# Optimization experiments

Measured on AMD Instinct MI355X. Metric: run time of the kernel, lower is better.

## Reference

```python
import jax, jax.numpy as jnp
import numpy as np

B, N, C = 4, 2047, 1024
H = 16
D = C // H  # head_dim = 64
SCALE = D ** -0.5


def setup_inputs() -> dict:
    key = jax.random.key(0)
    ks = jax.random.split(key, 5)
    return {
        "x": jax.random.normal(ks[0], (B, N, C), dtype=jnp.float32),
        "qkv_w": jax.random.normal(ks[1], (3 * C, C), dtype=jnp.float32) * (C ** -0.5),
        "proj_w": jax.random.normal(ks[2], (C, C), dtype=jnp.float32) * (C ** -0.5),
        "proj_b": jax.random.normal(ks[3], (C,), dtype=jnp.float32) * 0.02,
        "bias": jax.random.normal(ks[4], (H, N, N), dtype=jnp.float32) * 0.02,
    }


def reference(x, qkv_w, proj_w, proj_b, bias):
    b, n, c = x.shape
    qkv = (x @ qkv_w.T).reshape(b, n, 3, H, D)
    qkv = jnp.transpose(qkv, (2, 0, 3, 1, 4))
    q, k, v = qkv[0], qkv[1], qkv[2]
    q = q * SCALE
    # scores (B,H,N,N) + additive relative-position bias (H,N,N)
    attn = jnp.einsum('bhnd,bhmd->bhnm', q, k) + bias[None]
    attn = jax.nn.softmax(attn, axis=-1)
    out = jnp.einsum('bhnm,bhmd->bhnd', attn, v)
    out = jnp.transpose(out, (0, 2, 1, 3)).reshape(b, n, c)
    return out @ proj_w.T + proj_b
```

## Files before the change

kernel.cpp:

```cpp
#include <hip/hip_runtime.h>
#include <hip/hip_bf16.h>

typedef __bf16 bf16;
typedef __attribute__((ext_vector_type(8))) __bf16 bf16x8;
typedef __attribute__((ext_vector_type(4))) __bf16 bf16x4;
typedef __attribute__((ext_vector_type(4))) float f32x4;

#define MFMA16(a, b, c) __builtin_amdgcn_mfma_f32_16x16x32_bf16((a), (b), (c), 0, 0, 0)

constexpr int Bb = 4, Nn = 2047, Cc = 1024, Hh = 16, Dd = 64;
constexpr int M_ROWS = Bb * Nn;
constexpr int NPAD = 2048;
constexpr float SCALE = 0.125f;
constexpr float NEG_BIG = -1e30f;

__device__ inline bf16x8 bzero8() {
    bf16x8 v;
    for (int i = 0; i < 8; ++i) v[i] = (bf16)0.0f;
    return v;
}
__device__ inline bf16x8 bones8() {
    bf16x8 v;
    for (int i = 0; i < 8; ++i) v[i] = (bf16)1.0f;
    return v;
}
__device__ inline f32x4 fzero4() {
    f32x4 v = {0.f, 0.f, 0.f, 0.f};
    return v;
}

__device__ __forceinline__ void async_copy16(const void* g, void* l) {
    __builtin_amdgcn_global_load_lds(
        (const __attribute__((address_space(1))) unsigned int*)g,
        (__attribute__((address_space(3))) unsigned int*)l, 16, 0, 0);
}

__global__ __launch_bounds__(256) void cvt3_kernel(
    const float* __restrict__ a, bf16* __restrict__ oa, int na8,
    const float* __restrict__ b, bf16* __restrict__ ob, int nb8,
    const float* __restrict__ c, bf16* __restrict__ oc, int nc8) {
    int i = blockIdx.x * blockDim.x + threadIdx.x;
    const float* src;
    bf16* dst;
    int j = i;
    if (j < na8) {
        src = a; dst = oa;
    } else {
        j -= na8;
        if (j < nb8) {
            src = b; dst = ob;
        } else {
            j -= nb8;
            if (j >= nc8) return;
            src = c; dst = oc;
        }
    }
    float4 x0 = ((const float4*)src)[2 * (size_t)j];
    float4 x1 = ((const float4*)src)[2 * (size_t)j + 1];
    bf16x8 v;
    v[0] = (bf16)x0.x; v[1] = (bf16)x0.y; v[2] = (bf16)x0.z; v[3] = (bf16)x0.w;
    v[4] = (bf16)x1.x; v[5] = (bf16)x1.y; v[6] = (bf16)x1.z; v[7] = (bf16)x1.w;
    *(bf16x8*)(dst + 8 * (size_t)j) = v;
}

__global__ __launch_bounds__(256) void transpose_v_kernel(
    const bf16* __restrict__ vd, bf16* __restrict__ vtd) {
    __shared__ bf16 t[64 * 72];
    const int bh = blockIdx.x, nt = blockIdx.y;
    const int tid = threadIdx.x;
    const bf16* src = vd + (size_t)bh * Nn * Dd;
    bf16* dst = vtd + (size_t)bh * Dd * NPAD;
    int c = tid;
    for (int it = 0; it < 2; ++it, c += 256) {
        int row = c >> 3, d8 = (c & 7) * 8;
        int gn = nt * 64 + row;
        bf16x8 v = bzero8();
        if (gn < Nn) v = *(const bf16x8*)(src + (size_t)gn * Dd + d8);
        *(bf16x8*)(t + row * 72 + d8) = v;
    }
    __syncthreads();
    c = tid;
    for (int it = 0; it < 2; ++it, c += 256) {
        int d = c >> 3, j8 = (c & 7) * 8;
        bf16x8 v;
        for (int k = 0; k < 8; ++k) v[k] = t[(j8 + k) * 72 + d];
        *(bf16x8*)(dst + (size_t)d * NPAD + nt * 64 + j8) = v;
    }
}

template <int NOUT, int MODE>
__global__ __launch_bounds__(256, 2) void gemm_kernel(
    const bf16* __restrict__ A, const bf16* __restrict__ W,
    const float* __restrict__ pb, bf16* __restrict__ qd, bf16* __restrict__ kd,
    bf16* __restrict__ vd, float* __restrict__ outd) {
    constexpr int Kdim = 1024;
    __shared__ bf16 As[128 * 32];
    __shared__ bf16 Bs[128 * 32];

    const int tid = threadIdx.x;
    const int wave = tid >> 6, lane = tid & 63;
    const int quad = lane >> 4, l16 = lane & 15;
    const int m0 = blockIdx.y * 128;
    const int n0 = blockIdx.x * 128;
    const int wm = (wave >> 1) * 64, wn = (wave & 1) * 64;

    const int dma_r = lane >> 2;
    const int dma_k = (lane & 3) * 8;

    f32x4 acc[4][4];
    for (int mi = 0; mi < 4; ++mi)
        for (int ni = 0; ni < 4; ++ni) acc[mi][ni] = fzero4();

    for (int kb = 0; kb < Kdim; kb += 32) {
        __syncthreads();
        for (int i = 0; i < 2; ++i) {
            int g = wave * 2 + i;
            int row = g * 16 + dma_r;
            int gm = m0 + row;
            if (gm > M_ROWS - 1) gm = M_ROWS - 1;
            async_copy16(A + (size_t)gm * Kdim + kb + dma_k, As + g * 16 * 32);
        }
        for (int i = 0; i < 2; ++i) {
            int g = wave * 2 + i;
            int row = g * 16 + dma_r;
            async_copy16(W + (size_t)(n0 + row) * Kdim + kb + dma_k,
                         Bs + g * 16 * 32);
        }
        __syncthreads();

        bf16x8 af[4], bfr[4];
        for (int mi = 0; mi < 4; ++mi)
            af[mi] = *(const bf16x8*)(As + (wm + mi * 16 + l16) * 32 + quad * 8);
        for (int ni = 0; ni < 4; ++ni)
            bfr[ni] = *(const bf16x8*)(Bs + (wn + ni * 16 + l16) * 32 + quad * 8);
        for (int mi = 0; mi < 4; ++mi)
            for (int ni = 0; ni < 4; ++ni)
                acc[mi][ni] = MFMA16(af[mi], bfr[ni], acc[mi][ni]);
    }

    for (int mi = 0; mi < 4; ++mi) {
        for (int r = 0; r < 4; ++r) {
            int gm = m0 + wm + mi * 16 + quad * 4 + r;
            if (gm >= M_ROWS) continue;
            int bb = gm / Nn;
            int nn = gm - bb * Nn;
            for (int ni = 0; ni < 4; ++ni) {
                int gn = n0 + wn + ni * 16 + l16;
                float val = acc[mi][ni][r];
                if (MODE == 0) {
                    int which = gn >> 10;
                    int hh = (gn >> 6) & 15;
                    int dd = gn & 63;
                    size_t dst = ((size_t)(bb * Hh + hh) * Nn + nn) * Dd + dd;
                    if (which == 0)
                        qd[dst] = (bf16)(val * SCALE);
                    else if (which == 1)
                        kd[dst] = (bf16)val;
                    else
                        vd[dst] = (bf16)val;
                } else {
                    outd[(size_t)gm * NOUT + gn] = val + pb[gn];
                }
            }
        }
    }
}

__global__ __launch_bounds__(256, 4) void attn_kernel(
    const bf16* __restrict__ q, const bf16* __restrict__ kk,
    const bf16* __restrict__ vt, const float* __restrict__ bias,
    bf16* __restrict__ out) {
    __shared__ bf16 Qs[64 * 72];
    __shared__ bf16 Ks[64 * 72];
    __shared__ bf16 VTs[64 * 72];
    __shared__ bf16 Ps[64 * 72];

    const int tid = threadIdx.x;
    const int wave = tid >> 6, lane = tid & 63;
    const int quad = lane >> 4, l16 = lane & 15;

    const int flat = blockIdx.x;
    const int xcd = flat & 7;
    const int sidx = flat >> 3;
    const int pair = xcd * 64 + (sidx >> 2);
    const int b = sidx & 3;
    const int qt = pair & 31;
    const int h = pair >> 5;

    const int q0 = qt * 64;
    const int wq0 = wave * 16;

    const size_t head_off = (size_t)(b * Hh + h) * Nn * Dd;
    const bf16* qh = q + head_off;
    const bf16* kh = kk + head_off;
    const bf16* vth = vt + (size_t)(b * Hh + h) * Dd * NPAD;

    int gq_lane = q0 + wq0 + l16;
    if (gq_lane > Nn - 1) gq_lane = Nn - 1;
    const float* brow = bias + ((size_t)h * Nn + gq_lane) * Nn;

    const int srow = tid >> 3;
    const int sd8 = (tid & 7) * 8;

    {
        int c = tid;
        for (int it = 0; it < 2; ++it, c += 256) {
            int row = c >> 3, d8 = (c & 7) * 8;
            bf16x8 vq = bzero8();
            int gq = q0 + row;
            if (gq < Nn) vq = *(const bf16x8*)(qh + (size_t)gq * Dd + d8);
            *(bf16x8*)(Qs + row * 72 + d8) = vq;
        }
    }
    __syncthreads();
    const bf16x8 bq0 = *(const bf16x8*)(Qs + (wq0 + l16) * 72 + quad * 8);
    const bf16x8 bq1 = *(const bf16x8*)(Qs + (wq0 + l16) * 72 + 32 + quad * 8);
    const bf16x8 ones = bones8();

    bf16x8 pk0, pk1, pv0, pv1;
    float4 bp0, bp1, bp2, bp3;

    auto issue_kv = [&](int kvn) {
        int g0 = kvn + srow, g1 = kvn + srow + 32;
        pk0 = bzero8();
        pk1 = bzero8();
        if (g0 < Nn) pk0 = *(const bf16x8*)(kh + (size_t)g0 * Dd + sd8);
        if (g1 < Nn) pk1 = *(const bf16x8*)(kh + (size_t)g1 * Dd + sd8);
        pv0 = *(const bf16x8*)(vth + (size_t)srow * NPAD + kvn + sd8);
        pv1 = *(const bf16x8*)(vth + (size_t)(srow + 32) * NPAD + kvn + sd8);
    };
    auto issue_bias = [&](int tn) {
        const int kvn = tn * 64;
        if (tn < 31) {
            bp0 = *(const float4*)(brow + kvn + 0 * 16 + quad * 4);
            bp1 = *(const float4*)(brow + kvn + 1 * 16 + quad * 4);
            bp2 = *(const float4*)(brow + kvn + 2 * 16 + quad * 4);
            bp3 = *(const float4*)(brow + kvn + 3 * 16 + quad * 4);
        } else {
            float4 f[4];
            for (int mi = 0; mi < 4; ++mi) {
                int base = kvn + mi * 16 + quad * 4;
                f[mi].x = (base + 0 < Nn) ? brow[base + 0] : 0.f;
                f[mi].y = (base + 1 < Nn) ? brow[base + 1] : 0.f;
                f[mi].z = (base + 2 < Nn) ? brow[base + 2] : 0.f;
                f[mi].w = (base + 3 < Nn) ? brow[base + 3] : 0.f;
            }
            bp0 = f[0]; bp1 = f[1]; bp2 = f[2]; bp3 = f[3];
        }
    };

    issue_kv(0);
    issue_bias(0);

    f32x4 acc_o[4];
    for (int nd = 0; nd < 4; ++nd) acc_o[nd] = fzero4();
    f32x4 acc_l = fzero4();
    float m_prev = NEG_BIG;

    for (int t = 0; t < 32; ++t) {
        const int kv0 = t * 64;
        __syncthreads();

        *(bf16x8*)(Ks + srow * 72 + sd8) = pk0;
        *(bf16x8*)(Ks + (srow + 32) * 72 + sd8) = pk1;
        *(bf16x8*)(VTs + srow * 72 + sd8) = pv0;
        *(bf16x8*)(VTs + (srow + 32) * 72 + sd8) = pv1;

        float bv[4][4];
        bv[0][0] = bp0.x; bv[0][1] = bp0.y; bv[0][2] = bp0.z; bv[0][3] = bp0.w;
        bv[1][0] = bp1.x; bv[1][1] = bp1.y; bv[1][2] = bp1.z; bv[1][3] = bp1.w;
        bv[2][0] = bp2.x; bv[2][1] = bp2.y; bv[2][2] = bp2.z; bv[2][3] = bp2.w;
        bv[3][0] = bp3.x; bv[3][1] = bp3.y; bv[3][2] = bp3.z; bv[3][3] = bp3.w;

        __syncthreads();

        if (t < 31) {
            issue_kv(kv0 + 64);
            issue_bias(t + 1);
        }

        f32x4 sT[4];
        for (int mi = 0; mi < 4; ++mi) sT[mi] = fzero4();
        __builtin_amdgcn_s_setprio(1);
        for (int mi = 0; mi < 4; ++mi) {
            bf16x8 ak0 = *(const bf16x8*)(Ks + (mi * 16 + l16) * 72 + quad * 8);
            bf16x8 ak1 = *(const bf16x8*)(Ks + (mi * 16 + l16) * 72 + 32 + quad * 8);
            sT[mi] = MFMA16(ak0, bq0, sT[mi]);
            sT[mi] = MFMA16(ak1, bq1, sT[mi]);
        }
        __builtin_amdgcn_s_setprio(0);

        float s[4][4];
        for (int mi = 0; mi < 4; ++mi)
            for (int r = 0; r < 4; ++r) {
                int kv = kv0 + mi * 16 + quad * 4 + r;
                s[mi][r] = (kv < Nn) ? sT[mi][r] + bv[mi][r] : NEG_BIG;
            }

        float mx = s[0][0];
        for (int mi = 0; mi < 4; ++mi)
            for (int r = 0; r < 4; ++r) mx = fmaxf(mx, s[mi][r]);
        mx = fmaxf(mx, __shfl_xor(mx, 16));
        mx = fmaxf(mx, __shfl_xor(mx, 32));
        float mnew = fmaxf(m_prev, mx);
        float alpha_col = __expf(m_prev - mnew);
        m_prev = mnew;

        for (int mi = 0; mi < 4; ++mi) {
            bf16x4 pv;
            for (int r = 0; r < 4; ++r)
                pv[r] = (bf16)__expf(s[mi][r] - mnew);
            *(bf16x4*)(Ps + (wq0 + l16) * 72 + mi * 16 + quad * 4) = pv;
        }

        float ar[4];
        for (int r = 0; r < 4; ++r) ar[r] = __shfl(alpha_col, quad * 4 + r);
        for (int nd = 0; nd < 4; ++nd)
            for (int r = 0; r < 4; ++r) acc_o[nd][r] *= ar[r];
        for (int r = 0; r < 4; ++r) acc_l[r] *= ar[r];

        bf16x8 ap0 = *(const bf16x8*)(Ps + (wq0 + l16) * 72 + quad * 8);
        bf16x8 ap1 = *(const bf16x8*)(Ps + (wq0 + l16) * 72 + 32 + quad * 8);
        __builtin_amdgcn_s_setprio(1);
        for (int nd = 0; nd < 4; ++nd) {
            bf16x8 bv0 = *(const bf16x8*)(VTs + (nd * 16 + l16) * 72 + quad * 8);
            bf16x8 bv1 = *(const bf16x8*)(VTs + (nd * 16 + l16) * 72 + 32 + quad * 8);
            acc_o[nd] = MFMA16(ap0, bv0, acc_o[nd]);
            acc_o[nd] = MFMA16(ap1, bv1, acc_o[nd]);
        }
        acc_l = MFMA16(ap0, ones, acc_l);
        acc_l = MFMA16(ap1, ones, acc_l);
        __builtin_amdgcn_s_setprio(0);
    }

    for (int nd = 0; nd < 4; ++nd) {
        for (int r = 0; r < 4; ++r) {
            int gq = q0 + wq0 + quad * 4 + r;
            if (gq >= Nn) continue;
            float val = acc_o[nd][r] / acc_l[r];
            out[((size_t)b * Nn + gq) * Cc + h * 64 + nd * 16 + l16] = (bf16)val;
        }
    }
}

extern "C" void kernel_launch(void* const* d_in, const int* in_sizes, int n_in,
                              void* d_out, int out_size, void* d_ws,
                              size_t ws_size, hipStream_t stream) {
    const float* x = (const float*)d_in[0];
    const float* qkv_w = (const float*)d_in[1];
    const float* proj_w = (const float*)d_in[2];
    const float* proj_b = (const float*)d_in[3];
    const float* bias = (const float*)d_in[4];
    float* out = (float*)d_out;

    const size_t per = (size_t)Bb * Hh * Nn * Dd;
    const size_t nx = (size_t)M_ROWS * Cc;
    const size_t nqw = (size_t)3 * Cc * Cc;
    const size_t npw = (size_t)Cc * Cc;

    bf16* qkvwb = (bf16*)d_ws;
    bf16* projwb = qkvwb + nqw;
    bf16* qd = projwb + npw;
    bf16* kd = qd + per;
    bf16* vd = kd + per;
    bf16* ao = vd + per;
    bf16* xb = ao + nx;
    bf16* vtd = ao + nx;

    {
        int na8 = (int)(nx / 8), nb8 = (int)(nqw / 8), nc8 = (int)(npw / 8);
        int tot = na8 + nb8 + nc8;
        cvt3_kernel<<<(tot + 255) / 256, 256, 0, stream>>>(
            x, xb, na8, qkv_w, qkvwb, nb8, proj_w, projwb, nc8);
    }
    gemm_kernel<3072, 0><<<dim3(24, 64), 256, 0, stream>>>(
        xb, qkvwb, nullptr, qd, kd, vd, nullptr);
    transpose_v_kernel<<<dim3(64, 32), 256, 0, stream>>>(vd, vtd);
    attn_kernel<<<dim3(2048), 256, 0, stream>>>(qd, kd, vtd, bias, ao);
    gemm_kernel<1024, 1><<<dim3(8, 64), 256, 0, stream>>>(
        ao, projwb, proj_b, nullptr, nullptr, nullptr, out);
}
```

Before: 633.6 us.

## Defer softmax rescaling, fold bias into MFMA accumulator, peel last KV tile

The attention kernel now seeds the QK^T MFMA accumulator with the bias values instead of adding them afterwards. It peels the final KV tile into a compile-time-specialised path so the bounds checks and masking only run there. It also uses a deferred-max trick: the running max and the rescale of the accumulators are updated only when some lane's max grows by more than a threshold. Q is loaded directly from global memory into registers, dropping the Qs shared buffer and one barrier, and launch bounds are raised to 5 blocks per CU. Deferring the max trades fewer exp/shuffle/multiply operations for a larger range in the bf16 P values, which could hurt accuracy.

```diff
diff --git a/kernel.cpp b/kernel.cpp
--- a/kernel.cpp
+++ b/kernel.cpp
@@ -13,6 +13,9 @@
 constexpr int NPAD = 2048;
 constexpr float SCALE = 0.125f;
 constexpr float NEG_BIG = -1e30f;
+constexpr float DEFER_THR = 8.0f;
+
+template <bool V> struct BC { static constexpr bool value = V; };
 
 __device__ inline bf16x8 bzero8() {
     bf16x8 v;
@@ -166,11 +169,10 @@
     }
 }
 
-__global__ __launch_bounds__(256, 4) void attn_kernel(
+__global__ __launch_bounds__(256, 5) void attn_kernel(
     const bf16* __restrict__ q, const bf16* __restrict__ kk,
     const bf16* __restrict__ vt, const float* __restrict__ bias,
     bf16* __restrict__ out) {
-    __shared__ bf16 Qs[64 * 72];
     __shared__ bf16 Ks[64 * 72];
     __shared__ bf16 VTs[64 * 72];
     __shared__ bf16 Ps[64 * 72];
@@ -202,26 +204,23 @@
     const int srow = tid >> 3;
     const int sd8 = (tid & 7) * 8;
 
-    {
-        int c = tid;
-        for (int it = 0; it < 2; ++it, c += 256) {
-            int row = c >> 3, d8 = (c & 7) * 8;
-            bf16x8 vq = bzero8();
-            int gq = q0 + row;
-            if (gq < Nn) vq = *(const bf16x8*)(qh + (size_t)gq * Dd + d8);
-            *(bf16x8*)(Qs + row * 72 + d8) = vq;
-        }
-    }
-    __syncthreads();
-    const bf16x8 bq0 = *(const bf16x8*)(Qs + (wq0 + l16) * 72 + quad * 8);
-    const bf16x8 bq1 = *(const bf16x8*)(Qs + (wq0 + l16) * 72 + 32 + quad * 8);
+    const bf16* qrow = qh + (size_t)gq_lane * Dd;
+    const bf16x8 bq0 = *(const bf16x8*)(qrow + quad * 8);
+    const bf16x8 bq1 = *(const bf16x8*)(qrow + 32 + quad * 8);
     const bf16x8 ones = bones8();
 
     bf16x8 pk0, pk1, pv0, pv1;
-    float4 bp0, bp1, bp2, bp3;
-
-    auto issue_kv = [&](int kvn) {
-        int g0 = kvn + srow, g1 = kvn + srow + 32;
+    float4 bp[4];
+
+    auto issue_kv_fast = [&](int kvn) {
+        int g0 = kvn + srow, g1 = g0 + 32;
+        pk0 = *(const bf16x8*)(kh + (size_t)g0 * Dd + sd8);
+        pk1 = *(const bf16x8*)(kh + (size_t)g1 * Dd + sd8);
+        pv0 = *(const bf16x8*)(vth + (size_t)srow * NPAD + kvn + sd8);
+        pv1 = *(const bf16x8*)(vth + (size_t)(srow + 32) * NPAD + kvn + sd8);
+    };
+    auto issue_kv_last = [&](int kvn) {
+        int g0 = kvn + srow, g1 = g0 + 32;
         pk0 = bzero8();
         pk1 = bzero8();
         if (g0 < Nn) pk0 = *(const bf16x8*)(kh + (size_t)g0 * Dd + sd8);
@@ -232,32 +231,31 @@
     auto issue_bias = [&](int tn) {
         const int kvn = tn * 64;
         if (tn < 31) {
-            bp0 = *(const float4*)(brow + kvn + 0 * 16 + quad * 4);
-            bp1 = *(const float4*)(brow + kvn + 1 * 16 + quad * 4);
-            bp2 = *(const float4*)(brow + kvn + 2 * 16 + quad * 4);
-            bp3 = *(const float4*)(brow + kvn + 3 * 16 + quad * 4);
+            for (int mi = 0; mi < 4; ++mi)
+                bp[mi] = *(const float4*)(brow + kvn + mi * 16 + quad * 4);
         } else {
-            float4 f[4];
             for (int mi = 0; mi < 4; ++mi) {
                 int base = kvn + mi * 16 + quad * 4;
-                f[mi].x = (base + 0 < Nn) ? brow[base + 0] : 0.f;
-                f[mi].y = (base + 1 < Nn) ? brow[base + 1] : 0.f;
-                f[mi].z = (base + 2 < Nn) ? brow[base + 2] : 0.f;
-                f[mi].w = (base + 3 < Nn) ? brow[base + 3] : 0.f;
+                float4 f;
+                f.x = (base + 0 < Nn) ? brow[base + 0] : 0.f;
+                f.y = (base + 1 < Nn) ? brow[base + 1] : 0.f;
+                f.z = (base + 2 < Nn) ? brow[base + 2] : 0.f;
+                f.w = (base + 3 < Nn) ? brow[base + 3] : 0.f;
+                bp[mi] = f;
             }
-            bp0 = f[0]; bp1 = f[1]; bp2 = f[2]; bp3 = f[3];
         }
     };
 
-    issue_kv(0);
+    issue_kv_fast(0);
     issue_bias(0);
 
     f32x4 acc_o[4];
     for (int nd = 0; nd < 4; ++nd) acc_o[nd] = fzero4();
     f32x4 acc_l = fzero4();
-    float m_prev = NEG_BIG;
-
-    for (int t = 0; t < 32; ++t) {
+    float m_run = NEG_BIG;
+
+    auto tile = [&](int t, auto lastc) {
+        constexpr bool LAST = decltype(lastc)::value;
         const int kv0 = t * 64;
         __syncthreads();
 
@@ -266,26 +264,26 @@
         *(bf16x8*)(VTs + srow * 72 + sd8) = pv0;
         *(bf16x8*)(VTs + (srow + 32) * 72 + sd8) = pv1;
 
-        float bv[4][4];
-        bv[0][0] = bp0.x; bv[0][1] = bp0.y; bv[0][2] = bp0.z; bv[0][3] = bp0.w;
-        bv[1][0] = bp1.x; bv[1][1] = bp1.y; bv[1][2] = bp1.z; bv[1][3] = bp1.w;
-        bv[2][0] = bp2.x; bv[2][1] = bp2.y; bv[2][2] = bp2.z; bv[2][3] = bp2.w;
-        bv[3][0] = bp3.x; bv[3][1] = bp3.y; bv[3][2] = bp3.z; bv[3][3] = bp3.w;
+        f32x4 cin[4];
+        for (int mi = 0; mi < 4; ++mi) {
+            cin[mi][0] = bp[mi].x; cin[mi][1] = bp[mi].y;
+            cin[mi][2] = bp[mi].z; cin[mi][3] = bp[mi].w;
+        }
 
         __syncthreads();
 
-        if (t < 31) {
-            issue_kv(kv0 + 64);
+        if (!LAST) {
+            if (t + 1 < 31) issue_kv_fast(kv0 + 64);
+            else issue_kv_last(kv0 + 64);
             issue_bias(t + 1);
         }
 
         f32x4 sT[4];
-        for (int mi = 0; mi < 4; ++mi) sT[mi] = fzero4();
         __builtin_amdgcn_s_setprio(1);
         for (int mi = 0; mi < 4; ++mi) {
             bf16x8 ak0 = *(const bf16x8*)(Ks + (mi * 16 + l16) * 72 + quad * 8);
             bf16x8 ak1 = *(const bf16x8*)(Ks + (mi * 16 + l16) * 72 + 32 + quad * 8);
-            sT[mi] = MFMA16(ak0, bq0, sT[mi]);
+            sT[mi] = MFMA16(ak0, bq0, cin[mi]);
             sT[mi] = MFMA16(ak1, bq1, sT[mi]);
         }
         __builtin_amdgcn_s_setprio(0);
@@ -293,8 +291,12 @@
         float s[4][4];
         for (int mi = 0; mi < 4; ++mi)
             for (int r = 0; r < 4; ++r) {
-                int kv = kv0 + mi * 16 + quad * 4 + r;
-                s[mi][r] = (kv < Nn) ? sT[mi][r] + bv[mi][r] : NEG_BIG;
+                if (LAST) {
+                    int kv = kv0 + mi * 16 + quad * 4 + r;
+                    s[mi][r] = (kv < Nn) ? sT[mi][r] : NEG_BIG;
+                } else {
+                    s[mi][r] = sT[mi][r];
+                }
             }
 
         float mx = s[0][0];
@@ -302,22 +304,27 @@
             for (int r = 0; r < 4; ++r) mx = fmaxf(mx, s[mi][r]);
         mx = fmaxf(mx, __shfl_xor(mx, 16));
         mx = fmaxf(mx, __shfl_xor(mx, 32));
-        float mnew = fmaxf(m_prev, mx);
-        float alpha_col = __expf(m_prev - mnew);
-        m_prev = mnew;
+        float mnew = fmaxf(m_run, mx);
+
+        float m_old = m_run;
+        bool need = !__all(mnew - m_run <= DEFER_THR);
+        if (need) m_run = mnew;
 
         for (int mi = 0; mi < 4; ++mi) {
             bf16x4 pv;
             for (int r = 0; r < 4; ++r)
-                pv[r] = (bf16)__expf(s[mi][r] - mnew);
+                pv[r] = (bf16)__expf(s[mi][r] - m_run);
             *(bf16x4*)(Ps + (wq0 + l16) * 72 + mi * 16 + quad * 4) = pv;
         }
 
-        float ar[4];
-        for (int r = 0; r < 4; ++r) ar[r] = __shfl(alpha_col, quad * 4 + r);
-        for (int nd = 0; nd < 4; ++nd)
-            for (int r = 0; r < 4; ++r) acc_o[nd][r] *= ar[r];
-        for (int r = 0; r < 4; ++r) acc_l[r] *= ar[r];
+        if (need) {
+            float alpha_col = __expf(m_old - m_run);
+            float ar[4];
+            for (int r = 0; r < 4; ++r) ar[r] = __shfl(alpha_col, quad * 4 + r);
+            for (int nd = 0; nd < 4; ++nd)
+                for (int r = 0; r < 4; ++r) acc_o[nd][r] *= ar[r];
+            for (int r = 0; r < 4; ++r) acc_l[r] *= ar[r];
+        }
 
         bf16x8 ap0 = *(const bf16x8*)(Ps + (wq0 + l16) * 72 + quad * 8);
         bf16x8 ap1 = *(const bf16x8*)(Ps + (wq0 + l16) * 72 + 32 + quad * 8);
@@ -331,7 +338,10 @@
         acc_l = MFMA16(ap0, ones, acc_l);
         acc_l = MFMA16(ap1, ones, acc_l);
         __builtin_amdgcn_s_setprio(0);
-    }
+    };
+
+    for (int t = 0; t < 31; ++t) tile(t, BC<false>{});
+    tile(31, BC<true>{});
 
     for (int nd = 0; nd < 4; ++nd) {
         for (int r = 0; r < 4; ++r) {
```

After: 826.1 us. 1.3x slower.
